# Kernel tuning notes

Hardware: AMD Instinct MI355X
Metric: run time of the kernel (lower is better)

The kernel has to match this reference:

```python
import jax, jax.numpy as jnp
import numpy as np

NUM_HEADS = 16
EMBED_DIM = 1024
HEAD_DIM = EMBED_DIM // NUM_HEADS
REG_LEN = 2048
SUM_LEN = 64
BSZ = 2
REL_DIM = 64
NUM_REL_EMB = 64
MAX_SUMMARY = 64
SCALE = HEAD_DIM ** -0.5


def _ln(x, g, b, eps=1e-5):
    m = jnp.mean(x, axis=-1, keepdims=True)
    v = jnp.mean((x - m) ** 2, axis=-1, keepdims=True)
    return (x - m) * jax.lax.rsqrt(v + eps) * g + b


def setup_inputs() -> dict:
    key = jax.random.key(0)
    ks = jax.random.split(key, 16)
    inp = {}
    inp['reg_x'] = jax.random.normal(ks[0], (REG_LEN, BSZ, EMBED_DIM), jnp.float32)
    inp['sum_token_ids'] = jax.random.randint(ks[1], (BSZ, SUM_LEN), 0, MAX_SUMMARY + 1)
    inp['rel_idx'] = jax.random.randint(ks[2], (BSZ, SUM_LEN + REG_LEN, REG_LEN), 0, NUM_REL_EMB)
    inp['sum_len'] = SUM_LEN
    inp['reg_len'] = REG_LEN
    emb = jax.random.normal(ks[3], (MAX_SUMMARY + 1, EMBED_DIM), jnp.float32) * 0.02
    inp['emb_sum'] = emb.at[0].set(0.0)  # padding_idx = 0
    inp['rel_emb0'] = jax.random.normal(ks[4], (NUM_REL_EMB, REL_DIM), jnp.float32) * 0.02

    def lin(k, din, dout):
        return jax.random.normal(k, (din, dout), jnp.float32) * (1.0 / np.sqrt(din))

    inp['Wq'] = lin(ks[5], EMBED_DIM, EMBED_DIM); inp['bq'] = jnp.zeros((EMBED_DIM,), jnp.float32)
    inp['Wk'] = lin(ks[6], EMBED_DIM, EMBED_DIM); inp['bk'] = jnp.zeros((EMBED_DIM,), jnp.float32)
    inp['Wv'] = lin(ks[7], EMBED_DIM, EMBED_DIM); inp['bv'] = jnp.zeros((EMBED_DIM,), jnp.float32)
    inp['Wr0'] = lin(ks[8], REL_DIM, EMBED_DIM); inp['br0'] = jnp.zeros((EMBED_DIM,), jnp.float32)
    inp['Wk2'] = lin(ks[9], HEAD_DIM, HEAD_DIM); inp['bk2'] = jnp.zeros((HEAD_DIM,), jnp.float32)
    inp['Wv2'] = lin(ks[10], HEAD_DIM, HEAD_DIM); inp['bv2'] = jnp.zeros((HEAD_DIM,), jnp.float32)
    inp['Wo'] = lin(ks[11], EMBED_DIM, EMBED_DIM); inp['bo'] = jnp.zeros((EMBED_DIM,), jnp.float32)
    for name in ['ln_k', 'ln_v', 'ln_k2', 'ln_v2']:
        inp[name + '_g'] = jnp.ones((HEAD_DIM,), jnp.float32)
        inp[name + '_b'] = jnp.zeros((HEAD_DIM,), jnp.float32)
    return inp


def reference(reg_x, sum_token_ids, rel_idx, sum_len, reg_len, emb_sum, rel_emb0,
              Wq, bq, Wk, bk, Wv, bv, Wr0, br0, Wk2, bk2, Wv2, bv2, Wo, bo,
              ln_k_g, ln_k_b, ln_v_g, ln_v_b, ln_k2_g, ln_k2_b, ln_v2_g, ln_v2_b):
    R, B, E = reg_x.shape  # reg_len, bsz, embed_dim
    H, D = NUM_HEADS, HEAD_DIM
    S = sum_token_ids.shape[1]

    # regular K/V projections + per-head LayerNorm
    reg_k = _ln((reg_x @ Wk + bk).reshape(R, B, H, D), ln_k_g, ln_k_b)
    reg_v = _ln((reg_x @ Wv + bv).reshape(R, B, H, D), ln_v_g, ln_v_b)

    # relation-type embedding projection -> [Rrel, H, D]
    r0 = (rel_emb0 @ Wr0 + br0).reshape(NUM_REL_EMB, H, D)

    # --- stage 1: summary tokens attend over regular tokens ---
    sum_x = emb_sum[sum_token_ids.T]                     # [S, B, E]
    sum_q = sum_x.reshape(S, B, H, D) * SCALE
    scores_sum = jnp.einsum('sbhd,kbhd->bhsk', sum_q, reg_k)   # [B,H,S,R]
    qr_sum = jnp.einsum('sbhd,Zhd->bhsZ', sum_q, r0)           # [B,H,S,Rrel]
    idx_sum = rel_idx[:, :S]                                   # [B,S,R]
    scores_sum = scores_sum + jnp.take_along_axis(qr_sum, idx_sum[:, None, :, :], axis=-1)
    w_sum = jax.nn.softmax(scores_sum, axis=-1)
    sum_x2 = jnp.einsum('bhsk,kbhd->sbhd', w_sum, reg_v)       # [S,B,H,D]

    sum_k2 = _ln(sum_x2 @ Wk2 + bk2, ln_k2_g, ln_k2_b)
    sum_v2 = _ln(sum_x2 @ Wv2 + bv2, ln_v2_g, ln_v2_b)

    # --- stage 2: regular tokens attend over [summary ; regular] keys ---
    reg_q = (reg_x @ Wq + bq).reshape(R, B, H, D) * SCALE
    scores_rs = jnp.einsum('qbhd,sbhd->bhqs', reg_q, sum_k2)   # [B,H,R,S]
    scores_rr = jnp.einsum('qbhd,kbhd->bhqk', reg_q, reg_k)    # [B,H,R,R]
    qr_reg = jnp.einsum('qbhd,Zhd->bhqZ', reg_q, r0)
    idx_reg = rel_idx[:, S:]                                   # [B,R,R]
    scores_rr = scores_rr + jnp.take_along_axis(qr_reg, idx_reg[:, None, :, :], axis=-1)
    scores = jnp.concatenate([scores_rs, scores_rr], axis=-1)  # [B,H,R,S+R]
    w = jax.nn.softmax(scores, axis=-1)
    v_all = jnp.concatenate([sum_v2, reg_v], axis=0)           # [S+R,B,H,D]
    attn_out = jnp.einsum('bhqk,kbhd->qbhd', w, v_all).reshape(R, B, E)
    reg_x2 = attn_out @ Wo + bo
    return reg_x2
```

## Files before the change

kernel.cpp:

```cpp
#include <hip/hip_runtime.h>
#include <cstdint>
#include <cstddef>

#define NH   16
#define HD   64
#define RLEN 2048
#define BSZ  2
#define SLEN 64
#define NZ   64
#define ED   1024
#define KTOT 2112
#define NSPLIT 8

typedef __bf16 bf16_t;
typedef bf16_t bf16x8 __attribute__((ext_vector_type(8)));
typedef bf16_t bf16x4 __attribute__((ext_vector_type(4)));
typedef float  f32x4  __attribute__((ext_vector_type(4)));

__device__ __forceinline__ f32x4 mfma16(bf16x8 a, bf16x8 b, f32x4 c) {
    return __builtin_amdgcn_mfma_f32_16x16x32_bf16(a, b, c, 0, 0, 0);
}

__device__ __forceinline__ void dma16(const void* g, void* l) {
    __builtin_amdgcn_global_load_lds(
        (const __attribute__((address_space(1))) unsigned int*)g,
        (__attribute__((address_space(3))) unsigned int*)l, 16, 0, 0);
}


template<int BM>
__global__ __launch_bounds__(256) void gemm_fast(
    const bf16_t* __restrict__ A, const bf16_t* __restrict__ Bt,
    const float* __restrict__ b0, const float* __restrict__ b1,
    const float* __restrict__ b2,
    bf16_t* __restrict__ oq, float* __restrict__ o1, float* __restrict__ o2,
    int M, int K, int N, int mode)
{
    constexpr int MT = BM / 64;
    __shared__ __align__(16) bf16_t As[BM * 64];
    __shared__ __align__(16) bf16_t Bs[128 * 64];

    const int t = threadIdx.x;
    const int wave = t >> 6, lane = t & 63;
    const int quad = lane >> 4, l15 = lane & 15;
    const int rsub = lane >> 3, gq = lane & 7;
    const int m0 = blockIdx.y * BM, n0 = blockIdx.x * 128;

    f32x4 acc[MT][8];
#pragma unroll
    for (int i = 0; i < MT; i++)
#pragma unroll
        for (int j = 0; j < 8; j++) acc[i][j] = (f32x4){0.f, 0.f, 0.f, 0.f};

    for (int k0 = 0; k0 < K; k0 += 64) {
#pragma unroll
        for (int j = 0; j < BM / 32; j++) {
            int row = wave * (BM / 4) + j * 8 + rsub;
            const bf16_t* g = A + (size_t)(m0 + row) * K + k0 + ((gq ^ (row & 7)) * 8);
            dma16(g, As + (wave * (BM / 4) + j * 8) * 64);
        }
#pragma unroll
        for (int j = 0; j < 4; j++) {
            int row = wave * 32 + j * 8 + rsub;
            const bf16_t* g = Bt + (size_t)(n0 + row) * K + k0 + ((gq ^ (row & 7)) * 8);
            dma16(g, Bs + (wave * 32 + j * 8) * 64);
        }
        __syncthreads();

#pragma unroll
        for (int kk = 0; kk < 2; kk++) {
            const int pg = ((kk * 4 + quad) ^ (l15 & 7)) * 8;
            bf16x8 af[MT], bf[8];
#pragma unroll
            for (int mt = 0; mt < MT; mt++)
                af[mt] = *(const bf16x8*)(As + (wave * (BM / 4) + mt * 16 + l15) * 64 + pg);
#pragma unroll
            for (int nt = 0; nt < 8; nt++)
                bf[nt] = *(const bf16x8*)(Bs + (nt * 16 + l15) * 64 + pg);
#pragma unroll
            for (int mt = 0; mt < MT; mt++)
#pragma unroll
                for (int nt = 0; nt < 8; nt++)
                    acc[mt][nt] = mfma16(af[mt], bf[nt], acc[mt][nt]);
        }
        __syncthreads();
    }

#pragma unroll
    for (int mt = 0; mt < MT; mt++)
#pragma unroll
        for (int nt = 0; nt < 8; nt++)
#pragma unroll
            for (int reg = 0; reg < 4; reg++) {
                int m = m0 + wave * (BM / 4) + mt * 16 + quad * 4 + reg;
                int n = n0 + nt * 16 + l15;
                if (mode == 0) {
                    o1[(size_t)m * N + n] = acc[mt][nt][reg] + b0[n];
                } else {
                    int seg = n >> 10, nl = n & 1023;
                    const float* bias = (seg == 0) ? b0 : (seg == 1) ? b1 : b2;
                    float c = acc[mt][nt][reg] + bias[nl];
                    int h = nl >> 6, d = nl & 63;
                    int r = m >> 1, bb = m & 1;
                    size_t off = (((size_t)bb * NH + h) * RLEN + r) * HD + d;
                    if (seg == 0)      oq[off] = (bf16_t)(c * 0.125f);
                    else if (seg == 1) o1[off] = c;
                    else               o2[off] = c;
                }
            }
}

__global__ __launch_bounds__(256) void gemm_mfma(
    const bf16_t* __restrict__ A, const bf16_t* __restrict__ Bt,
    const float* __restrict__ bias, float* __restrict__ outf,
    int M, int K, int N, int Rr)
{
    constexpr int LDA = 40;
    __shared__ __align__(16) bf16_t As[64 * LDA];
    __shared__ __align__(16) bf16_t Bs[128 * LDA];

    const int t = threadIdx.x;
    const int wave = t >> 6, lane = t & 63;
    const int quad = lane >> 4, l15 = lane & 15;
    const int wrow = wave >> 1, wcol = wave & 1;
    const int m0 = blockIdx.y * 64, n0 = blockIdx.x * 128;

    f32x4 acc[2][4];
#pragma unroll
    for (int i = 0; i < 2; i++)
#pragma unroll
        for (int j = 0; j < 4; j++) acc[i][j] = (f32x4){0.f, 0.f, 0.f, 0.f};

    const int srow = t >> 2, sseg = (t & 3) * 8;

    for (int k0 = 0; k0 < K; k0 += 32) {
        bf16x8 av  = *(const bf16x8*)(A  + (size_t)(m0 + srow) * K + k0 + sseg);
        bf16x8 bv0 = *(const bf16x8*)(Bt + (size_t)(n0 + srow) * K + k0 + sseg);
        bf16x8 bv1 = *(const bf16x8*)(Bt + (size_t)(n0 + 64 + srow) * K + k0 + sseg);
        __syncthreads();
        *(bf16x8*)(As + srow * LDA + sseg)        = av;
        *(bf16x8*)(Bs + srow * LDA + sseg)        = bv0;
        *(bf16x8*)(Bs + (64 + srow) * LDA + sseg) = bv1;
        __syncthreads();

        bf16x8 af[2], bf[4];
#pragma unroll
        for (int mt = 0; mt < 2; mt++)
            af[mt] = *(const bf16x8*)(As + (wrow * 32 + mt * 16 + l15) * LDA + quad * 8);
#pragma unroll
        for (int nt = 0; nt < 4; nt++)
            bf[nt] = *(const bf16x8*)(Bs + (wcol * 64 + nt * 16 + l15) * LDA + quad * 8);
#pragma unroll
        for (int mt = 0; mt < 2; mt++)
#pragma unroll
            for (int nt = 0; nt < 4; nt++)
                acc[mt][nt] = mfma16(af[mt], bf[nt], acc[mt][nt]);
    }

#pragma unroll
    for (int mt = 0; mt < 2; mt++)
#pragma unroll
        for (int nt = 0; nt < 4; nt++)
#pragma unroll
            for (int reg = 0; reg < 4; reg++) {
                int m = m0 + wrow * 32 + mt * 16 + quad * 4 + reg;
                int n = n0 + wcol * 64 + nt * 16 + l15;
                if (m >= M) continue;
                float c = acc[mt][nt][reg] + bias[n];
                int h = n >> 6, d = n & 63;
                outf[(((size_t)h) * Rr + m) * HD + d] = c;
            }
}

__global__ __launch_bounds__(256) void ln_k_frag(
    const float* __restrict__ x, const float* __restrict__ g, const float* __restrict__ b,
    bf16_t* __restrict__ kfm)
{
    int row  = blockIdx.x * 4 + (threadIdx.x >> 6);
    int lane = threadIdx.x & 63;
    float v = x[(size_t)row * HD + lane];
    float s1 = v, s2 = v * v;
#pragma unroll
    for (int o = 32; o > 0; o >>= 1) {
        s1 += __shfl_xor(s1, o);
        s2 += __shfl_xor(s2, o);
    }
    float mean = s1 * (1.f / 64.f);
    float var  = s2 * (1.f / 64.f) - mean * mean;
// ... 7 lines not shown

__global__ __launch_bounds__(256) void lnv_frag(
    const float* __restrict__ v, const float* __restrict__ g,
    const float* __restrict__ b, bf16_t* __restrict__ vfm)
{
    __shared__ float tile[64][65];
    const int bh = blockIdx.y, tidx = blockIdx.x;
    const int t = threadIdx.x;
    const int wave = t >> 6, lane = t & 63;

#pragma unroll
    for (int i = 0; i < 16; i++) {
        int rl = wave * 16 + i;
        float x = v[((size_t)bh * RLEN + tidx * 64 + rl) * HD + lane];
        float s1 = x, s2 = x * x;
#pragma unroll
        for (int o = 32; o > 0; o >>= 1) {
            s1 += __shfl_xor(s1, o);
            s2 += __shfl_xor(s2, o);
        }
        float mean = s1 * (1.f / 64.f);
        float var  = s2 * (1.f / 64.f) - mean * mean;
        tile[rl][lane] = (x - mean) * rsqrtf(var + 1e-5f) * g[lane] + b[lane];
    }
    __syncthreads();
    int d = t >> 2, rs = (t & 3) * 16;
    bf16x8 o0, o1;
#pragma unroll
    for (int j = 0; j < 8; j++) {
        o0[j] = (bf16_t)tile[rs + j][d];
        o1[j] = (bf16_t)tile[rs + 8 + j][d];
    }
    size_t base = (size_t)bh * 131072;
    size_t off0 = base + (size_t)((((tidx * 4 + (d >> 4)) * 2 + (rs >> 5)) * 64
                  + ((rs >> 3) & 3) * 16 + (d & 15)) * 8);
    int rs2 = rs + 8;
    size_t off1 = base + (size_t)((((tidx * 4 + (d >> 4)) * 2 + (rs2 >> 5)) * 64
                  + ((rs2 >> 3) & 3) * 16 + (d & 15)) * 8);
    *(bf16x8*)(vfm + off0) = o0;
    *(bf16x8*)(vfm + off1) = o1;
}

__global__ __launch_bounds__(256) void cvt_bf16(
    const float* __restrict__ src, bf16_t* __restrict__ dst, int n)
{
    int i = (blockIdx.x * 256 + threadIdx.x) * 4;
    if (i < n) {
        float4 v = *(const float4*)(src + i);
        bf16x4 o;
        o[0] = (bf16_t)v.x; o[1] = (bf16_t)v.y; o[2] = (bf16_t)v.z; o[3] = (bf16_t)v.w;
        *(bf16x4*)(dst + i) = o;
    }
}

__global__ __launch_bounds__(256) void prep_batch(
    const float* __restrict__ Wq, const float* __restrict__ Wk,
    const float* __restrict__ Wv, const float* __restrict__ Wo,
    const float* __restrict__ Wr0,
    bf16_t* __restrict__ wqt, bf16_t* __restrict__ wkt,
    bf16_t* __restrict__ wvt, bf16_t* __restrict__ wot,
    bf16_t* __restrict__ wr0t,
    const float* __restrict__ emb, const int* __restrict__ ids,
    bf16_t* __restrict__ sum_q,
    const float* __restrict__ rel_emb0, bf16_t* __restrict__ re0b)
{
    const int bid = blockIdx.x;
    const int t = threadIdx.x;

    if (bid >= 1168) {
        int i = ((bid - 1168) * 256 + t) * 4;
        float4 v = *(const float4*)(rel_emb0 + i);
        bf16x4 o;
        o[0] = (bf16_t)v.x; o[1] = (bf16_t)v.y; o[2] = (bf16_t)v.z; o[3] = (bf16_t)v.w;
        *(bf16x4*)(re0b + i) = o;
        return;
    }
    if (bid >= 1040) {
        int sb = bid - 1040;
        int s = sb >> 1, b = sb & 1;
        int id = ids[b * SLEN + s];
        const float* src = emb + (size_t)id * ED;
        for (int e = t; e < ED; e += 256) {
            int h = e >> 6, d = e & 63;
            sum_q[(((size_t)b * NH + h) * SLEN + s) * HD + d] = (bf16_t)(src[e] * 0.125f);
        }
        return;
    }

    __shared__ float tile[64][65];
    const float* src; bf16_t* dst; int R, C, r0, c0;
    if (bid < 1024) {
        int sel = bid >> 8, local = bid & 255;
        src = (sel == 0) ? Wq : (sel == 1) ? Wk : (sel == 2) ? Wv : Wo;
        dst = (sel == 0) ? wqt : (sel == 1) ? wkt : (sel == 2) ? wvt : wot;
        R = ED; C = ED; r0 = (local >> 4) * 64; c0 = (local & 15) * 64;
    } else {
        src = Wr0; dst = wr0t; R = NZ; C = ED; r0 = 0; c0 = (bid - 1024) * 64;
    }
#pragma unroll
    for (int i = 0; i < 4; i++) {
        int idx = t + i * 256;
        int r = idx >> 4, c = (idx & 15) * 4;
        float4 vv = *(const float4*)(src + (size_t)(r0 + r) * C + c0 + c);
        tile[r][c] = vv.x; tile[r][c + 1] = vv.y; tile[r][c + 2] = vv.z; tile[r][c + 3] = vv.w;
    }
    __syncthreads();
    int cc = t >> 2, rs = (t & 3) * 16;
    bf16x8 o0, o1;
#pragma unroll
    for (int j = 0; j < 8; j++) {
        o0[j] = (bf16_t)tile[rs + j][cc];
        o1[j] = (bf16_t)tile[rs + 8 + j][cc];
    }
    *(bf16x8*)(dst + (size_t)(c0 + cc) * R + r0 + rs) = o0;
    *(bf16x8*)(dst + (size_t)(c0 + cc) * R + r0 + rs + 8) = o1;
}

template<int MT>
__device__ __forceinline__ void attn_tile(
    const bf16_t* __restrict__ kt, const bf16_t* __restrict__ vt,
    const int* __restrict__ relbase, int koff, bool userel,
    const float* __restrict__ qrsw, bf16_t* __restrict__ Psw,
    const bf16x8 (&qf)[MT][2],
    f32x4 (&O)[MT][4], float& m_q, float (&l_i)[MT][4],
    int quad, int l15, int lane)
{
    bf16x8 kf[4][2];
#pragma unroll
    for (int nt = 0; nt < 4; nt++)
#pragma unroll
        for (int kb = 0; kb < 2; kb++)
            kf[nt][kb] = *(const bf16x8*)(kt + ((nt * 2 + kb) * 64 + lane) * 8);

    int4 crel[MT][4];
    if (userel) {
#pragma unroll
        for (int mt = 0; mt < MT; mt++)
#pragma unroll
            for (int reg = 0; reg < 4; reg++)
                crel[mt][reg] = *(const int4*)(relbase + (size_t)(mt * 16 + reg) * RLEN + koff);
    }

    f32x4 S[MT][4];
#pragma unroll
    for (int mt = 0; mt < MT; mt++)
#pragma unroll
        for (int nt = 0; nt < 4; nt++) {
            f32x4 acc = (f32x4){0.f, 0.f, 0.f, 0.f};
            acc = mfma16(qf[mt][0], kf[nt][0], acc);
            acc = mfma16(qf[mt][1], kf[nt][1], acc);
            S[mt][nt] = acc;
        }

    bf16x8 vf[4][2];
#pragma unroll
    for (int nt = 0; nt < 4; nt++)
#pragma unroll
        for (int kb = 0; kb < 2; kb++)
            vf[nt][kb] = *(const bf16x8*)(vt + ((nt * 2 + kb) * 64 + lane) * 8);

    if (userel) {
#pragma unroll
        for (int mt = 0; mt < MT; mt++)
#pragma unroll
            for (int reg = 0; reg < 4; reg++) {
                const float* qr = qrsw + (mt * 16 + quad * 4 + reg) * 64;
                int4 c = crel[mt][reg];
                S[mt][0][reg] += qr[c.x];
                S[mt][1][reg] += qr[c.y];
                S[mt][2][reg] += qr[c.z];
                S[mt][3][reg] += qr[c.w];
            }
    }

    float v = -1e30f;
#pragma unroll
    for (int mt = 0; mt < MT; mt++)
#pragma unroll
        for (int nt = 0; nt < 4; nt++) {
            f32x4 s = S[mt][nt];
            v = fmaxf(v, fmaxf(fmaxf(s[0], s[1]), fmaxf(s[2], s[3])));
        }
#pragma unroll
    for (int o = 8; o > 0; o >>= 1) v = fmaxf(v, __shfl_xor(v, o));
    float mnew = fmaxf(m_q, v);
    float alpha = __expf(m_q - mnew);
    m_q = mnew;

#pragma unroll
    for (int mt = 0; mt < MT; mt++)
#pragma unroll
        for (int nt = 0; nt < 4; nt++)
#pragma unroll
            for (int reg = 0; reg < 4; reg++)
                S[mt][nt][reg] = __expf(S[mt][nt][reg] - mnew);

#pragma unroll
    for (int mt = 0; mt < MT; mt++) {
#pragma unroll
        for (int nt = 0; nt < 4; nt++) {
            O[mt][nt][0] *= alpha; O[mt][nt][1] *= alpha;
            O[mt][nt][2] *= alpha; O[mt][nt][3] *= alpha;
        }
#pragma unroll
        for (int reg = 0; reg < 4; reg++) l_i[mt][reg] *= alpha;
    }

    bf16x8 ones;
#pragma unroll
    for (int j = 0; j < 8; j++) ones[j] = (bf16_t)1.0f;

#pragma unroll
    for (int mt = 0; mt < MT; mt++)
#pragma unroll
        for (int reg = 0; reg < 4; reg++) {
            bf16x4 pv;
            pv[0] = (bf16_t)S[mt][0][reg]; pv[1] = (bf16_t)S[mt][1][reg];
            pv[2] = (bf16_t)S[mt][2][reg]; pv[3] = (bf16_t)S[mt][3][reg];
            *(bf16x4*)(Psw + (mt * 16 + quad * 4 + reg) * 72 + 4 * l15) = pv;
        }

#pragma unroll
    for (int mt = 0; mt < MT; mt++) {
        bf16x8 pf0 = *(const bf16x8*)(Psw + (mt * 16 + l15) * 72 + quad * 8);
        bf16x8 pf1 = *(const bf16x8*)(Psw + (mt * 16 + l15) * 72 + 32 + quad * 8);
        f32x4 ls = (f32x4){0.f, 0.f, 0.f, 0.f};
        ls = mfma16(pf0, ones, ls);
        ls = mfma16(pf1, ones, ls);
#pragma unroll
        for (int nt = 0; nt < 4; nt++) {
            O[mt][nt] = mfma16(pf0, vf[nt][0], O[mt][nt]);
            O[mt][nt] = mfma16(pf1, vf[nt][1], O[mt][nt]);
        }
#pragma unroll
        for (int reg = 0; reg < 4; reg++) l_i[mt][reg] += ls[reg];
    }
}

template<int MT>
__device__ __forceinline__ void build_qr(
    const float* __restrict__ r0, int h, const bf16x8 (&qf)[MT][2],
    float* __restrict__ qrsw, int quad, int l15)
{
#pragma unroll
    for (int nt = 0; nt < 4; nt++) {
        const float* rp = r0 + ((size_t)h * NZ + l15 + 16 * nt) * HD + quad * 8;
        float4 a0 = *(const float4*)(rp);
        float4 a1 = *(const float4*)(rp + 4);
        bf16x8 bf0;
        bf0[0] = (bf16_t)a0.x; bf0[1] = (bf16_t)a0.y; bf0[2] = (bf16_t)a0.z; bf0[3] = (bf16_t)a0.w;
        bf0[4] = (bf16_t)a1.x; bf0[5] = (bf16_t)a1.y; bf0[6] = (bf16_t)a1.z; bf0[7] = (bf16_t)a1.w;
        float4 b0 = *(const float4*)(rp + 32);
        float4 b1 = *(const float4*)(rp + 36);
        bf16x8 bf1;
        bf1[0] = (bf16_t)b0.x; bf1[1] = (bf16_t)b0.y; bf1[2] = (bf16_t)b0.z; bf1[3] = (bf16_t)b0.w;
        bf1[4] = (bf16_t)b1.x; bf1[5] = (bf16_t)b1.y; bf1[6] = (bf16_t)b1.z; bf1[7] = (bf16_t)b1.w;
#pragma unroll
        for (int mt = 0; mt < MT; mt++) {
            f32x4 qa = (f32x4){0.f, 0.f, 0.f, 0.f};
            qa = mfma16(qf[mt][0], bf0, qa);
            qa = mfma16(qf[mt][1], bf1, qa);
#pragma unroll
            for (int reg = 0; reg < 4; reg++)
                qrsw[(mt * 16 + quad * 4 + reg) * 64 + l15 + 16 * nt] = qa[reg];
        }
    }
}

__global__ __launch_bounds__(256) void sum_attn_split(
    const bf16_t* __restrict__ Qb,
    const bf16_t* __restrict__ kfm, const bf16_t* __restrict__ vfm,
    const float*  __restrict__ r0,
    const int*    __restrict__ rel_idx,
    float* __restrict__ po, float* __restrict__ pm, float* __restrict__ pl)
{
    const int bh = blockIdx.x;
    const int split = blockIdx.y;
    const int b = bh >> 4, h = bh & 15;
    const int t = threadIdx.x;
    const int wave = t >> 6, lane = t & 63;
    const int quad = lane >> 4, l15 = lane & 15;

    __shared__ __align__(16) bf16_t Ps[4][16 * 72];
    __shared__ float qrs[4][16 * 64];

    bf16x8 qf[1][2];
    const bf16_t* Qrow = Qb + ((size_t)bh * SLEN + wave * 16 + l15) * HD;
    qf[0][0] = *(const bf16x8*)(Qrow + quad * 8);
    qf[0][1] = *(const bf16x8*)(Qrow + 32 + quad * 8);

    build_qr<1>(r0, h, qf, qrs[wave], quad, l15);

    f32x4 O[1][4];
    float m_q = -1e30f;
    float l_i[1][4];
#pragma unroll
    for (int nt = 0; nt < 4; nt++) O[0][nt] = (f32x4){0.f, 0.f, 0.f, 0.f};
#pragma unroll
    for (int r = 0; r < 4; r++) l_i[0][r] = 0.f;

    const int* relbase = rel_idx + ((size_t)b * KTOT + wave * 16 + quad * 4) * RLEN + 4 * l15;

    const bf16_t* kbase = kfm + (size_t)bh * 131072 + (size_t)(split * 4) * 4096;
    const bf16_t* vbase = vfm + (size_t)bh * 131072 + (size_t)(split * 4) * 4096;

    for (int i = 0; i < 4; i++) {
        const int koff = (split * 4 + i) * 64;
        attn_tile<1>(kbase + (size_t)i * 4096, vbase + (size_t)i * 4096,
                     relbase, koff, true, qrs[wave], Ps[wave], qf,
                     O, m_q, l_i, quad, l15, lane);
    }

    const size_t pslot = (size_t)bh * NSPLIT + split;
#pragma unroll
    for (int nt = 0; nt < 4; nt++)
#pragma unroll
        for (int reg = 0; reg < 4; reg++) {
            int sq = wave * 16 + quad * 4 + reg;
            po[(pslot * SLEN + sq) * HD + l15 + 16 * nt] = O[0][nt][reg];
        }
#pragma unroll
    for (int reg = 0; reg < 4; reg++) {
        int sq = wave * 16 + quad * 4 + reg;
        if (l15 == 0) {
            pm[pslot * SLEN + sq] = m_q;
            pl[pslot * SLEN + sq] = l_i[0][reg];
        }
    }
}

__global__ __launch_bounds__(64) void k2v2_fused(
    const float* __restrict__ po, const float* __restrict__ pm,
    const float* __restrict__ pl,
    const float* __restrict__ Wk2, const float* __restrict__ bk2,
    const float* __restrict__ Wv2, const float* __restrict__ bv2,
    const float* __restrict__ gk, const float* __restrict__ bk,
    const float* __restrict__ gv, const float* __restrict__ bv,
    bf16_t* __restrict__ k2fm, bf16_t* __restrict__ v2fm)
{
    int row = blockIdx.x;
    int d = threadIdx.x;
    int bh = row >> 6, s = row & 63;

    float M = -1e30f, mm[NSPLIT];
#pragma unroll
    for (int j = 0; j < NSPLIT; j++) {
        mm[j] = pm[((size_t)bh * NSPLIT + j) * SLEN + s];
        M = fmaxf(M, mm[j]);
    }
    float L = 0.f, acc = 0.f;
#pragma unroll
    for (int j = 0; j < NSPLIT; j++) {
        float a = __expf(mm[j] - M);
        L += pl[((size_t)bh * NSPLIT + j) * SLEN + s] * a;
        acc += po[(((size_t)bh * NSPLIT + j) * SLEN + s) * HD + d] * a;
    }
    __shared__ float xs[64];
    xs[d] = acc / L;
    __syncthreads();

#pragma unroll
    for (int which = 0; which < 2; which++) {
        const float* W  = which ? Wv2 : Wk2;
        const float* bi = which ? bv2 : bk2;
        const float* g  = which ? gv : gk;
        const float* bb = which ? bv : bk;
        float a = bi[d];
#pragma unroll
        for (int j = 0; j < 64; j++) a += xs[j] * W[j * HD + d];
        float s1 = a, s2 = a * a;
#pragma unroll
        for (int o = 32; o > 0; o >>= 1) {
            s1 += __shfl_xor(s1, o);
            s2 += __shfl_xor(s2, o);
        }
        float mean = s1 * (1.f / 64.f);
        float var  = s2 * (1.f / 64.f) - mean * mean;
        float y = (a - mean) * rsqrtf(var + 1e-5f) * g[d] + bb[d];
        if (which == 0) {
            size_t off = (size_t)bh * 4096 +
                (size_t)((((s & 3) * 2 + (d >> 5)) * 64
                          + ((d >> 3) & 3) * 16 + (s >> 2)) * 8 + (d & 7));
            k2fm[off] = (bf16_t)y;
        } else {
            size_t off = (size_t)bh * 4096 +
                (size_t)((((d >> 4) * 2 + (s >> 5)) * 64
                          + ((s >> 3) & 3) * 16 + (d & 15)) * 8 + (s & 7));
            v2fm[off] = (bf16_t)y;
        }
    }
}

__global__ __launch_bounds__(256) void reg_attn_mfma(
    const bf16_t* __restrict__ Qb,
    const bf16_t* __restrict__ kfm, const bf16_t* __restrict__ vfm,
    const bf16_t* __restrict__ k2fm, const bf16_t* __restrict__ v2fm,
    const float*  __restrict__ r0,
    const int*    __restrict__ rel_idx,
    bf16_t* __restrict__ attn_out)
{
    const int bid = blockIdx.x;
    const int bh = (bid & 7) * 4 + ((bid >> 3) & 3);
    const int qt = bid >> 5;
    const int b = bh >> 4, h = bh & 15;
    const int q0 = qt * 128;

    const int t = threadIdx.x;
    const int wave = t >> 6, lane = t & 63;
    const int quad = lane >> 4, l15 = lane & 15;

    __shared__ __align__(16) bf16_t Ps[4][32 * 72];
    __shared__ float qrs[4][32 * 64];

    bf16x8 qf[2][2];
#pragma unroll
    for (int mt = 0; mt < 2; mt++) {
        const bf16_t* Qrow = Qb + ((size_t)bh * RLEN + q0 + wave * 32 + mt * 16 + l15) * HD;
        qf[mt][0] = *(const bf16x8*)(Qrow + quad * 8);
        qf[mt][1] = *(const bf16x8*)(Qrow + 32 + quad * 8);
    }

    build_qr<2>(r0, h, qf, qrs[wave], quad, l15);

    f32x4 O[2][4];
    float m_q = -1e30f;
    float l_i[2][4];
#pragma unroll
    for (int mt = 0; mt < 2; mt++)
#pragma unroll
        for (int nt = 0; nt < 4; nt++) O[mt][nt] = (f32x4){0.f, 0.f, 0.f, 0.f};
#pragma unroll
    for (int mt = 0; mt < 2; mt++)
#pragma unroll
        for (int r = 0; r < 4; r++) l_i[mt][r] = 0.f;

    const int* relbase = rel_idx +
        ((size_t)b * KTOT + SLEN + q0 + wave * 32 + quad * 4) * RLEN + 4 * l15;

    attn_tile<2>(k2fm + (size_t)bh * 4096, v2fm + (size_t)bh * 4096,
                 relbase, 0, false, qrs[wave], Ps[wave], qf,
                 O, m_q, l_i, quad, l15, lane);

    const bf16_t* kt = kfm + (size_t)bh * 131072;
    const bf16_t* vt = vfm + (size_t)bh * 131072;
    for (int tile = 0; tile < 32; tile++) {
        attn_tile<2>(kt, vt, relbase, tile * 64, true,
                     qrs[wave], Ps[wave], qf, O, m_q, l_i, quad, l15, lane);
        kt += 4096; vt += 4096;
    }

#pragma unroll
    for (int mt = 0; mt < 2; mt++) {
        float linv[4];
#pragma unroll
        for (int reg = 0; reg < 4; reg++) linv[reg] = 1.0f / l_i[mt][reg];
#pragma unroll
        for (int nt = 0; nt < 4; nt++)
#pragma unroll
            for (int reg = 0; reg < 4; reg++) {
                int q = q0 + wave * 32 + mt * 16 + quad * 4 + reg;
                attn_out[((size_t)q * BSZ + b) * ED + h * HD + l15 + 16 * nt] =
                    (bf16_t)(O[mt][nt][reg] * linv[reg]);
            }
    }
}

extern "C" void kernel_launch(void* const* d_in, const int* in_sizes, int n_in,
                              void* d_out, int out_size, void* d_ws, size_t ws_size,
                              hipStream_t stream)
{
    const float* reg_x    = (const float*)d_in[0];
    const int*   sum_ids  = (const int*)d_in[1];
    const int*   rel_idx  = (const int*)d_in[2];
    const float* emb_sum  = (const float*)d_in[5];
    const float* rel_emb0 = (const float*)d_in[6];
    const float* Wq = (const float*)d_in[7];
    const float* bq = (const float*)d_in[8];
    const float* Wk = (const float*)d_in[9];
    const float* bk = (const float*)d_in[10];
    const float* Wv = (const float*)d_in[11];
    const float* bv = (const float*)d_in[12];
    const float* Wr0 = (const float*)d_in[13];
    const float* br0 = (const float*)d_in[14];
    const float* Wk2 = (const float*)d_in[15];
    const float* bk2 = (const float*)d_in[16];
    const float* Wv2 = (const float*)d_in[17];
    const float* bv2 = (const float*)d_in[18];
    const float* Wo  = (const float*)d_in[19];
    const float* bo  = (const float*)d_in[20];
    const float* ln_k_g  = (const float*)d_in[21];
    const float* ln_k_b  = (const float*)d_in[22];
    const float* ln_v_g  = (const float*)d_in[23];
    const float* ln_v_b  = (const float*)d_in[24];
    const float* ln_k2_g = (const float*)d_in[25];
    const float* ln_k2_b = (const float*)d_in[26];
    const float* ln_v2_g = (const float*)d_in[27];
    const float* ln_v2_b = (const float*)d_in[28];

    const size_t QKV = (size_t)BSZ * NH * RLEN * HD;
    const size_t SUM = (size_t)BSZ * NH * SLEN * HD;

    float* ws  = (float*)d_ws;
    float* k   = ws;
    float* v   = k + QKV;
    float* r0  = v + QKV;

    bf16_t* xb   = (bf16_t*)(r0 + (size_t)NH * NZ * HD);
    bf16_t* qb   = xb + QKV;
    bf16_t* kfm  = qb + QKV;
    bf16_t* vfm  = kfm + QKV;
    bf16_t* sqb  = vfm + QKV;
    bf16_t* k2fm = sqb + SUM;
    bf16_t* v2fm = k2fm + SUM;
    bf16_t* wqt  = v2fm + SUM;
    bf16_t* wkt  = wqt + (size_t)ED * ED;
    bf16_t* wvt  = wkt + (size_t)ED * ED;
    bf16_t* wot  = wvt + (size_t)ED * ED;
    bf16_t* wr0t = wot + (size_t)ED * ED;
    bf16_t* re0b = wr0t + (size_t)ED * NZ;
    bf16_t* aob  = (bf16_t*)k;
    float*  po   = (float*)xb;
    float*  pm   = po + (size_t)BSZ * NH * NSPLIT * SLEN * HD;
    float*  pl   = pm + (size_t)BSZ * NH * NSPLIT * SLEN;

    const int M = RLEN * BSZ;

    cvt_bf16<<<(int)(QKV / 1024), 256, 0, stream>>>(reg_x, xb, (int)QKV);
    prep_batch<<<1172, 256, 0, stream>>>(Wq, Wk, Wv, Wo, Wr0,
                                         wqt, wkt, wvt, wot, wr0t,
                                         emb_sum, sum_ids, sqb, rel_emb0, re0b);

    gemm_fast<128><<<dim3(3 * ED / 128, M / 128), 256, 0, stream>>>(
        xb, wqt, bq, bk, bv, qb, k, v, M, ED, 3 * ED, 1);

    ln_k_frag<<<(BSZ * NH * RLEN) / 4, 256, 0, stream>>>(k, ln_k_g, ln_k_b, kfm);
    lnv_frag<<<dim3(RLEN / 64, BSZ * NH), 256, 0, stream>>>(v, ln_v_g, ln_v_b, vfm);

    gemm_mfma<<<dim3(ED / 128, 1), 256, 0, stream>>>(re0b, wr0t, br0, r0, NZ, NZ, ED, NZ);

    sum_attn_split<<<dim3(BSZ * NH, NSPLIT), 256, 0, stream>>>(sqb, kfm, vfm, r0, rel_idx, po, pm, pl);

    k2v2_fused<<<BSZ * NH * SLEN, 64, 0, stream>>>(po, pm, pl, Wk2, bk2, Wv2, bv2,
                                                   ln_k2_g, ln_k2_b, ln_v2_g, ln_v2_b,
                                                   k2fm, v2fm);

    reg_attn_mfma<<<512, 256, 0, stream>>>(qb, kfm, vfm, k2fm, v2fm, r0, rel_idx, aob);

    gemm_fast<64><<<dim3(ED / 128, M / 64), 256, 0, stream>>>(
        aob, wot, bo, nullptr, nullptr, nullptr, (float*)d_out, nullptr, M, ED, ED, 0);
}
```

Measured before the change: 371.0 us.

## Use exp2 softmax with lazy rescaling and finer-grained attention work split

The log2(e) factor is folded into the query scale so that all softmax exponentials use exp2f. The running-max rescale of O and l is skipped when the new tile max stays within 8 of the current max. The regular-attention kernel drops to one 16-row M tile per wave and launches twice as many blocks. The summary attention split count is doubled from 8 to 16, and its partial buffers move into the v workspace to make room. The aim is cheaper exponentials, less rescaling work and better GPU occupancy, at the cost of more K/V reloads per query and larger bf16 P values, up to 256, under lazy rescaling.

```diff
diff --git a/kernel.cpp b/kernel.cpp
--- a/kernel.cpp
+++ b/kernel.cpp
@@ -10,7 +10,9 @@
 #define NZ   64
 #define ED   1024
 #define KTOT 2112
-#define NSPLIT 8
+#define NSPLIT 16
+
+#define QSCALE 0.18033688011112042f
 
 typedef __bf16 bf16_t;
 typedef bf16_t bf16x8 __attribute__((ext_vector_type(8)));
@@ -103,7 +105,7 @@
                     int h = nl >> 6, d = nl & 63;
                     int r = m >> 1, bb = m & 1;
                     size_t off = (((size_t)bb * NH + h) * RLEN + r) * HD + d;
-                    if (seg == 0)      oq[off] = (bf16_t)(c * 0.125f);
+                    if (seg == 0)      oq[off] = (bf16_t)(c * QSCALE);
                     else if (seg == 1) o1[off] = c;
                     else               o2[off] = c;
                 }
@@ -277,7 +279,7 @@
         const float* src = emb + (size_t)id * ED;
         for (int e = t; e < ED; e += 256) {
             int h = e >> 6, d = e & 63;
-            sum_q[(((size_t)b * NH + h) * SLEN + s) * HD + d] = (bf16_t)(src[e] * 0.125f);
+            sum_q[(((size_t)b * NH + h) * SLEN + s) * HD + d] = (bf16_t)(src[e] * QSCALE);
         }
         return;
     }
@@ -378,9 +380,22 @@
         }
 #pragma unroll
     for (int o = 8; o > 0; o >>= 1) v = fmaxf(v, __shfl_xor(v, o));
-    float mnew = fmaxf(m_q, v);
-    float alpha = __expf(m_q - mnew);
-    m_q = mnew;
+
+    if (!__all(v <= m_q + 8.0f)) {
+        float mnew = fmaxf(m_q, v);
+        float alpha = exp2f(m_q - mnew);
+        m_q = mnew;
+#pragma unroll
+        for (int mt = 0; mt < MT; mt++) {
+#pragma unroll
+            for (int nt = 0; nt < 4; nt++) {
+                O[mt][nt][0] *= alpha; O[mt][nt][1] *= alpha;
+                O[mt][nt][2] *= alpha; O[mt][nt][3] *= alpha;
+            }
+#pragma unroll
+            for (int reg = 0; reg < 4; reg++) l_i[mt][reg] *= alpha;
+        }
+    }
 
 #pragma unroll
     for (int mt = 0; mt < MT; mt++)
@@ -388,18 +403,7 @@
         for (int nt = 0; nt < 4; nt++)
 #pragma unroll
             for (int reg = 0; reg < 4; reg++)
-                S[mt][nt][reg] = __expf(S[mt][nt][reg] - mnew);
-
-#pragma unroll
-    for (int mt = 0; mt < MT; mt++) {
-#pragma unroll
-        for (int nt = 0; nt < 4; nt++) {
-            O[mt][nt][0] *= alpha; O[mt][nt][1] *= alpha;
-            O[mt][nt][2] *= alpha; O[mt][nt][3] *= alpha;
-        }
-#pragma unroll
-        for (int reg = 0; reg < 4; reg++) l_i[mt][reg] *= alpha;
-    }
+                S[mt][nt][reg] = exp2f(S[mt][nt][reg] - m_q);
 
     bf16x8 ones;
 #pragma unroll
@@ -469,6 +473,7 @@
     const int*    __restrict__ rel_idx,
     float* __restrict__ po, float* __restrict__ pm, float* __restrict__ pl)
 {
+    constexpr int TPS = 32 / NSPLIT;
     const int bh = blockIdx.x;
     const int split = blockIdx.y;
     const int b = bh >> 4, h = bh & 15;
@@ -496,11 +501,11 @@
 
     const int* relbase = rel_idx + ((size_t)b * KTOT + wave * 16 + quad * 4) * RLEN + 4 * l15;
 
-    const bf16_t* kbase = kfm + (size_t)bh * 131072 + (size_t)(split * 4) * 4096;
-    const bf16_t* vbase = vfm + (size_t)bh * 131072 + (size_t)(split * 4) * 4096;
-
-    for (int i = 0; i < 4; i++) {
-        const int koff = (split * 4 + i) * 64;
+    const bf16_t* kbase = kfm + (size_t)bh * 131072 + (size_t)(split * TPS) * 4096;
+    const bf16_t* vbase = vfm + (size_t)bh * 131072 + (size_t)(split * TPS) * 4096;
+
+    for (int i = 0; i < TPS; i++) {
+        const int koff = (split * TPS + i) * 64;
         attn_tile<1>(kbase + (size_t)i * 4096, vbase + (size_t)i * 4096,
                      relbase, koff, true, qrs[wave], Ps[wave], qf,
                      O, m_q, l_i, quad, l15, lane);
@@ -546,7 +551,7 @@
     float L = 0.f, acc = 0.f;
 #pragma unroll
     for (int j = 0; j < NSPLIT; j++) {
-        float a = __expf(mm[j] - M);
+        float a = exp2f(mm[j] - M);
         L += pl[((size_t)bh * NSPLIT + j) * SLEN + s] * a;
         acc += po[(((size_t)bh * NSPLIT + j) * SLEN + s) * HD + d] * a;
     }
@@ -598,64 +603,58 @@
     const int bh = (bid & 7) * 4 + ((bid >> 3) & 3);
     const int qt = bid >> 5;
     const int b = bh >> 4, h = bh & 15;
-    const int q0 = qt * 128;
+    const int q0 = qt * 64;
 
     const int t = threadIdx.x;
     const int wave = t >> 6, lane = t & 63;
     const int quad = lane >> 4, l15 = lane & 15;
 
-    __shared__ __align__(16) bf16_t Ps[4][32 * 72];
-    __shared__ float qrs[4][32 * 64];
-
-    bf16x8 qf[2][2];
-#pragma unroll
-    for (int mt = 0; mt < 2; mt++) {
-        const bf16_t* Qrow = Qb + ((size_t)bh * RLEN + q0 + wave * 32 + mt * 16 + l15) * HD;
-        qf[mt][0] = *(const bf16x8*)(Qrow + quad * 8);
-        qf[mt][1] = *(const bf16x8*)(Qrow + 32 + quad * 8);
-    }
-
-    build_qr<2>(r0, h, qf, qrs[wave], quad, l15);
-
-    f32x4 O[2][4];
+    __shared__ __align__(16) bf16_t Ps[4][16 * 72];
+    __shared__ float qrs[4][16 * 64];
+
+    bf16x8 qf[1][2];
+    {
+        const bf16_t* Qrow = Qb + ((size_t)bh * RLEN + q0 + wave * 16 + l15) * HD;
+        qf[0][0] = *(const bf16x8*)(Qrow + quad * 8);
+        qf[0][1] = *(const bf16x8*)(Qrow + 32 + quad * 8);
+    }
+
+    build_qr<1>(r0, h, qf, qrs[wave], quad, l15);
+
+    f32x4 O[1][4];
     float m_q = -1e30f;
-    float l_i[2][4];
-#pragma unroll
-    for (int mt = 0; mt < 2; mt++)
-#pragma unroll
-        for (int nt = 0; nt < 4; nt++) O[mt][nt] = (f32x4){0.f, 0.f, 0.f, 0.f};
-#pragma unroll
-    for (int mt = 0; mt < 2; mt++)
-#pragma unroll
-        for (int r = 0; r < 4; r++) l_i[mt][r] = 0.f;
+    float l_i[1][4];
+#pragma unroll
+    for (int nt = 0; nt < 4; nt++) O[0][nt] = (f32x4){0.f, 0.f, 0.f, 0.f};
+#pragma unroll
+    for (int r = 0; r < 4; r++) l_i[0][r] = 0.f;
 
     const int* relbase = rel_idx +
-        ((size_t)b * KTOT + SLEN + q0 + wave * 32 + quad * 4) * RLEN + 4 * l15;
-
-    attn_tile<2>(k2fm + (size_t)bh * 4096, v2fm + (size_t)bh * 4096,
+        ((size_t)b * KTOT + SLEN + q0 + wave * 16 + quad * 4) * RLEN + 4 * l15;
+
+    attn_tile<1>(k2fm + (size_t)bh * 4096, v2fm + (size_t)bh * 4096,
                  relbase, 0, false, qrs[wave], Ps[wave], qf,
                  O, m_q, l_i, quad, l15, lane);
 
     const bf16_t* kt = kfm + (size_t)bh * 131072;
     const bf16_t* vt = vfm + (size_t)bh * 131072;
     for (int tile = 0; tile < 32; tile++) {
-        attn_tile<2>(kt, vt, relbase, tile * 64, true,
+        attn_tile<1>(kt, vt, relbase, tile * 64, true,
                      qrs[wave], Ps[wave], qf, O, m_q, l_i, quad, l15, lane);
         kt += 4096; vt += 4096;
     }
 
-#pragma unroll
-    for (int mt = 0; mt < 2; mt++) {
+    {
         float linv[4];
 #pragma unroll
-        for (int reg = 0; reg < 4; reg++) linv[reg] = 1.0f / l_i[mt][reg];
+        for (int reg = 0; reg < 4; reg++) linv[reg] = 1.0f / l_i[0][reg];
 #pragma unroll
         for (int nt = 0; nt < 4; nt++)
 #pragma unroll
             for (int reg = 0; reg < 4; reg++) {
-                int q = q0 + wave * 32 + mt * 16 + quad * 4 + reg;
+                int q = q0 + wave * 16 + quad * 4 + reg;
                 attn_out[((size_t)q * BSZ + b) * ED + h * HD + l15 + 16 * nt] =
-                    (bf16_t)(O[mt][nt][reg] * linv[reg]);
+                    (bf16_t)(O[0][nt][reg] * linv[reg]);
             }
     }
 }
@@ -714,7 +713,7 @@
     bf16_t* wr0t = wot + (size_t)ED * ED;
     bf16_t* re0b = wr0t + (size_t)ED * NZ;
     bf16_t* aob  = (bf16_t*)k;
-    float*  po   = (float*)xb;
+    float*  po   = v;
     float*  pm   = po + (size_t)BSZ * NH * NSPLIT * SLEN * HD;
     float*  pl   = pm + (size_t)BSZ * NH * NSPLIT * SLEN;
 
@@ -739,7 +738,7 @@
                                                    ln_k2_g, ln_k2_b, ln_v2_g, ln_v2_b,
                                                    k2fm, v2fm);
 
-    reg_attn_mfma<<<512, 256, 0, stream>>>(qb, kfm, vfm, k2fm, v2fm, r0, rel_idx, aob);
+    reg_attn_mfma<<<1024, 256, 0, stream>>>(qb, kfm, vfm, k2fm, v2fm, r0, rel_idx, aob);
 
     gemm_fast<64><<<dim3(ED / 128, M / 64), 256, 0, stream>>>(
         aob, wot, bo, nullptr, nullptr, nullptr, (float*)d_out, nullptr, M, ED, ED, 0);
```

Result: slower. 398.6 us (+7.4%).

## Split KV range across wave halves in reg attention and use exp2 lazy rescale

Applied to the files above, without the earlier changes.

The regular-token attention kernel now runs 8 waves per block. Two halves each process half of the key tiles for the same queries, then merge their partial max, sum and output through shared memory. Softmax switches to exp2, with log2(e) folded into the query scale, and skips rescaling of the accumulators when the running max grows by at most 8. The summary-attention split count doubles to 16, and its partial buffers move into the freed v workspace. These changes aim to raise parallelism and cut exp and rescale work, at the cost of extra block syncs, more shared memory and register pressure under the 512-thread launch bound.

```diff
diff --git a/kernel.cpp b/kernel.cpp
--- a/kernel.cpp
+++ b/kernel.cpp
@@ -10,7 +10,9 @@
 #define NZ   64
 #define ED   1024
 #define KTOT 2112
-#define NSPLIT 8
+#define NSPLIT 16
+
+#define QSCALE 0.18033688011112042f
 
 typedef __bf16 bf16_t;
 typedef bf16_t bf16x8 __attribute__((ext_vector_type(8)));
@@ -103,7 +105,7 @@
                     int h = nl >> 6, d = nl & 63;
                     int r = m >> 1, bb = m & 1;
                     size_t off = (((size_t)bb * NH + h) * RLEN + r) * HD + d;
-                    if (seg == 0)      oq[off] = (bf16_t)(c * 0.125f);
+                    if (seg == 0)      oq[off] = (bf16_t)(c * QSCALE);
                     else if (seg == 1) o1[off] = c;
                     else               o2[off] = c;
                 }
@@ -277,7 +279,7 @@
         const float* src = emb + (size_t)id * ED;
         for (int e = t; e < ED; e += 256) {
             int h = e >> 6, d = e & 63;
-            sum_q[(((size_t)b * NH + h) * SLEN + s) * HD + d] = (bf16_t)(src[e] * 0.125f);
+            sum_q[(((size_t)b * NH + h) * SLEN + s) * HD + d] = (bf16_t)(src[e] * QSCALE);
         }
         return;
     }
@@ -378,9 +380,22 @@
         }
 #pragma unroll
     for (int o = 8; o > 0; o >>= 1) v = fmaxf(v, __shfl_xor(v, o));
-    float mnew = fmaxf(m_q, v);
-    float alpha = __expf(m_q - mnew);
-    m_q = mnew;
+
+    if (!__all(v <= m_q + 8.0f)) {
+        float mnew = fmaxf(m_q, v);
+        float alpha = exp2f(m_q - mnew);
+        m_q = mnew;
+#pragma unroll
+        for (int mt = 0; mt < MT; mt++) {
+#pragma unroll
+            for (int nt = 0; nt < 4; nt++) {
+                O[mt][nt][0] *= alpha; O[mt][nt][1] *= alpha;
+                O[mt][nt][2] *= alpha; O[mt][nt][3] *= alpha;
+            }
+#pragma unroll
+            for (int reg = 0; reg < 4; reg++) l_i[mt][reg] *= alpha;
+        }
+    }
 
 #pragma unroll
     for (int mt = 0; mt < MT; mt++)
@@ -388,18 +403,7 @@
         for (int nt = 0; nt < 4; nt++)
 #pragma unroll
             for (int reg = 0; reg < 4; reg++)
-                S[mt][nt][reg] = __expf(S[mt][nt][reg] - mnew);
-
-#pragma unroll
-    for (int mt = 0; mt < MT; mt++) {
-#pragma unroll
-        for (int nt = 0; nt < 4; nt++) {
-            O[mt][nt][0] *= alpha; O[mt][nt][1] *= alpha;
-            O[mt][nt][2] *= alpha; O[mt][nt][3] *= alpha;
-        }
-#pragma unroll
-        for (int reg = 0; reg < 4; reg++) l_i[mt][reg] *= alpha;
-    }
+                S[mt][nt][reg] = exp2f(S[mt][nt][reg] - m_q);
 
     bf16x8 ones;
 #pragma unroll
@@ -469,6 +473,7 @@
     const int*    __restrict__ rel_idx,
     float* __restrict__ po, float* __restrict__ pm, float* __restrict__ pl)
 {
+    constexpr int TPS = 32 / NSPLIT;
     const int bh = blockIdx.x;
     const int split = blockIdx.y;
     const int b = bh >> 4, h = bh & 15;
@@ -496,11 +501,11 @@
 
     const int* relbase = rel_idx + ((size_t)b * KTOT + wave * 16 + quad * 4) * RLEN + 4 * l15;
 
-    const bf16_t* kbase = kfm + (size_t)bh * 131072 + (size_t)(split * 4) * 4096;
-    const bf16_t* vbase = vfm + (size_t)bh * 131072 + (size_t)(split * 4) * 4096;
-
-    for (int i = 0; i < 4; i++) {
-        const int koff = (split * 4 + i) * 64;
+    const bf16_t* kbase = kfm + (size_t)bh * 131072 + (size_t)(split * TPS) * 4096;
+    const bf16_t* vbase = vfm + (size_t)bh * 131072 + (size_t)(split * TPS) * 4096;
+
+    for (int i = 0; i < TPS; i++) {
+        const int koff = (split * TPS + i) * 64;
         attn_tile<1>(kbase + (size_t)i * 4096, vbase + (size_t)i * 4096,
                      relbase, koff, true, qrs[wave], Ps[wave], qf,
                      O, m_q, l_i, quad, l15, lane);
@@ -546,7 +551,7 @@
     float L = 0.f, acc = 0.f;
 #pragma unroll
     for (int j = 0; j < NSPLIT; j++) {
-        float a = __expf(mm[j] - M);
+        float a = exp2f(mm[j] - M);
         L += pl[((size_t)bh * NSPLIT + j) * SLEN + s] * a;
         acc += po[(((size_t)bh * NSPLIT + j) * SLEN + s) * HD + d] * a;
     }
@@ -586,7 +591,7 @@
     }
 }
 
-__global__ __launch_bounds__(256) void reg_attn_mfma(
+__global__ __launch_bounds__(512, 4) void reg_attn_mfma(
     const bf16_t* __restrict__ Qb,
     const bf16_t* __restrict__ kfm, const bf16_t* __restrict__ vfm,
     const bf16_t* __restrict__ k2fm, const bf16_t* __restrict__ v2fm,
@@ -602,20 +607,22 @@
 
     const int t = threadIdx.x;
     const int wave = t >> 6, lane = t & 63;
+    const int wq = wave & 3, half = wave >> 2;
     const int quad = lane >> 4, l15 = lane & 15;
 
-    __shared__ __align__(16) bf16_t Ps[4][32 * 72];
-    __shared__ float qrs[4][32 * 64];
+    __shared__ __align__(16) bf16_t Ps[8][32 * 72];
+    __shared__ __align__(16) float qrs[4][32 * 64];
+    __shared__ float msh[2][4][4];
 
     bf16x8 qf[2][2];
 #pragma unroll
     for (int mt = 0; mt < 2; mt++) {
-        const bf16_t* Qrow = Qb + ((size_t)bh * RLEN + q0 + wave * 32 + mt * 16 + l15) * HD;
+        const bf16_t* Qrow = Qb + ((size_t)bh * RLEN + q0 + wq * 32 + mt * 16 + l15) * HD;
         qf[mt][0] = *(const bf16x8*)(Qrow + quad * 8);
         qf[mt][1] = *(const bf16x8*)(Qrow + 32 + quad * 8);
     }
 
-    build_qr<2>(r0, h, qf, qrs[wave], quad, l15);
+    build_qr<2>(r0, h, qf, qrs[wq], quad, l15);
 
     f32x4 O[2][4];
     float m_q = -1e30f;
@@ -630,33 +637,65 @@
         for (int r = 0; r < 4; r++) l_i[mt][r] = 0.f;
 
     const int* relbase = rel_idx +
-        ((size_t)b * KTOT + SLEN + q0 + wave * 32 + quad * 4) * RLEN + 4 * l15;
-
-    attn_tile<2>(k2fm + (size_t)bh * 4096, v2fm + (size_t)bh * 4096,
-                 relbase, 0, false, qrs[wave], Ps[wave], qf,
-                 O, m_q, l_i, quad, l15, lane);
-
-    const bf16_t* kt = kfm + (size_t)bh * 131072;
-    const bf16_t* vt = vfm + (size_t)bh * 131072;
-    for (int tile = 0; tile < 32; tile++) {
-        attn_tile<2>(kt, vt, relbase, tile * 64, true,
-                     qrs[wave], Ps[wave], qf, O, m_q, l_i, quad, l15, lane);
+        ((size_t)b * KTOT + SLEN + q0 + wq * 32 + quad * 4) * RLEN + 4 * l15;
+
+    if (half == 0)
+        attn_tile<2>(k2fm + (size_t)bh * 4096, v2fm + (size_t)bh * 4096,
+                     relbase, 0, false, qrs[wq], Ps[wave], qf,
+                     O, m_q, l_i, quad, l15, lane);
+
+    const bf16_t* kt = kfm + (size_t)bh * 131072 + (size_t)(half * 16) * 4096;
+    const bf16_t* vt = vfm + (size_t)bh * 131072 + (size_t)(half * 16) * 4096;
+    for (int tile = 0; tile < 16; tile++) {
+        attn_tile<2>(kt, vt, relbase, (half * 16 + tile) * 64, true,
+                     qrs[wq], Ps[wave], qf, O, m_q, l_i, quad, l15, lane);
         kt += 4096; vt += 4096;
     }
 
-#pragma unroll
-    for (int mt = 0; mt < 2; mt++) {
-        float linv[4];
-#pragma unroll
-        for (int reg = 0; reg < 4; reg++) linv[reg] = 1.0f / l_i[mt][reg];
-#pragma unroll
-        for (int nt = 0; nt < 4; nt++)
-#pragma unroll
-            for (int reg = 0; reg < 4; reg++) {
-                int q = q0 + wave * 32 + mt * 16 + quad * 4 + reg;
-                attn_out[((size_t)q * BSZ + b) * ED + h * HD + l15 + 16 * nt] =
-                    (bf16_t)(O[mt][nt][reg] * linv[reg]);
-            }
+    msh[half][wq][quad] = m_q;
+    __syncthreads();
+    float mo = msh[1 - half][wq][quad];
+    float al = exp2f(m_q - fmaxf(m_q, mo));
+
+    if (half == 1) {
+        float* osh = qrs[wq];
+        float* lsh = (float*)(Ps[4 + wq]);
+#pragma unroll
+        for (int mt = 0; mt < 2; mt++) {
+#pragma unroll
+            for (int nt = 0; nt < 4; nt++)
+#pragma unroll
+                for (int reg = 0; reg < 4; reg++)
+                    osh[(mt * 16 + quad * 4 + reg) * 64 + l15 + 16 * nt] =
+                        O[mt][nt][reg] * al;
+            if (l15 == 0)
+#pragma unroll
+                for (int reg = 0; reg < 4; reg++)
+                    lsh[mt * 16 + quad * 4 + reg] = l_i[mt][reg] * al;
+        }
+    }
+    __syncthreads();
+    if (half == 0) {
+        const float* osh = qrs[wq];
+        const float* lsh = (const float*)(Ps[4 + wq]);
+#pragma unroll
+        for (int mt = 0; mt < 2; mt++) {
+            float linv[4];
+#pragma unroll
+            for (int reg = 0; reg < 4; reg++)
+                linv[reg] = 1.0f /
+                    (l_i[mt][reg] * al + lsh[mt * 16 + quad * 4 + reg]);
+#pragma unroll
+            for (int nt = 0; nt < 4; nt++)
+#pragma unroll
+                for (int reg = 0; reg < 4; reg++) {
+                    int q = q0 + wq * 32 + mt * 16 + quad * 4 + reg;
+                    float ot = O[mt][nt][reg] * al
+                             + osh[(mt * 16 + quad * 4 + reg) * 64 + l15 + 16 * nt];
+                    attn_out[((size_t)q * BSZ + b) * ED + h * HD + l15 + 16 * nt] =
+                        (bf16_t)(ot * linv[reg]);
+                }
+        }
     }
 }
 
@@ -714,7 +753,7 @@
     bf16_t* wr0t = wot + (size_t)ED * ED;
     bf16_t* re0b = wr0t + (size_t)ED * NZ;
     bf16_t* aob  = (bf16_t*)k;
-    float*  po   = (float*)xb;
+    float*  po   = v;
     float*  pm   = po + (size_t)BSZ * NH * NSPLIT * SLEN * HD;
     float*  pl   = pm + (size_t)BSZ * NH * NSPLIT * SLEN;
 
@@ -739,7 +778,7 @@
                                                    ln_k2_g, ln_k2_b, ln_v2_g, ln_v2_b,
                                                    k2fm, v2fm);
 
-    reg_attn_mfma<<<512, 256, 0, stream>>>(qb, kfm, vfm, k2fm, v2fm, r0, rel_idx, aob);
+    reg_attn_mfma<<<512, 512, 0, stream>>>(qb, kfm, vfm, k2fm, v2fm, r0, rel_idx, aob);
 
     gemm_fast<64><<<dim3(ED / 128, M / 64), 256, 0, stream>>>(
         aob, wot, bo, nullptr, nullptr, nullptr, (float*)d_out, nullptr, M, ED, ED, 0);
```

After: 480.3 us. 29.4% more time.

## Use exp2 softmax with lazy rescale, finer sum splits, single-wave reg attention blocks

Applied to the files above, without the earlier changes.

The softmax now works in base 2: log2(e) is folded into the query scale so exp2f replaces __expf, and the split-merge step is updated to match. The online-softmax rescale of O and l is skipped unless the running max grows by more than 8, which cuts per-tile multiplies and exp calls. The summary attention split count doubles from 8 to 16, with partials moved to the larger fp32 v buffer so they fit. Regular attention launches 2048 single-wave blocks of 32 queries instead of 512 four-wave blocks. This gives more independent blocks for scheduling, at the cost of more blocks each reloading the same K/V tiles.

```diff
diff --git a/kernel.cpp b/kernel.cpp
--- a/kernel.cpp
+++ b/kernel.cpp
@@ -10,7 +10,9 @@
 #define NZ   64
 #define ED   1024
 #define KTOT 2112
-#define NSPLIT 8
+#define NSPLIT 16
+
+#define QSCALE 0.18033688011112042f
 
 typedef __bf16 bf16_t;
 typedef bf16_t bf16x8 __attribute__((ext_vector_type(8)));
@@ -103,7 +105,7 @@
                     int h = nl >> 6, d = nl & 63;
                     int r = m >> 1, bb = m & 1;
                     size_t off = (((size_t)bb * NH + h) * RLEN + r) * HD + d;
-                    if (seg == 0)      oq[off] = (bf16_t)(c * 0.125f);
+                    if (seg == 0)      oq[off] = (bf16_t)(c * QSCALE);
                     else if (seg == 1) o1[off] = c;
                     else               o2[off] = c;
                 }
@@ -277,7 +279,7 @@
         const float* src = emb + (size_t)id * ED;
         for (int e = t; e < ED; e += 256) {
             int h = e >> 6, d = e & 63;
-            sum_q[(((size_t)b * NH + h) * SLEN + s) * HD + d] = (bf16_t)(src[e] * 0.125f);
+            sum_q[(((size_t)b * NH + h) * SLEN + s) * HD + d] = (bf16_t)(src[e] * QSCALE);
         }
         return;
     }
@@ -378,9 +380,22 @@
         }
 #pragma unroll
     for (int o = 8; o > 0; o >>= 1) v = fmaxf(v, __shfl_xor(v, o));
-    float mnew = fmaxf(m_q, v);
-    float alpha = __expf(m_q - mnew);
-    m_q = mnew;
+
+    if (!__all(v <= m_q + 8.0f)) {
+        float mnew = fmaxf(m_q, v);
+        float alpha = exp2f(m_q - mnew);
+        m_q = mnew;
+#pragma unroll
+        for (int mt = 0; mt < MT; mt++) {
+#pragma unroll
+            for (int nt = 0; nt < 4; nt++) {
+                O[mt][nt][0] *= alpha; O[mt][nt][1] *= alpha;
+                O[mt][nt][2] *= alpha; O[mt][nt][3] *= alpha;
+            }
+#pragma unroll
+            for (int reg = 0; reg < 4; reg++) l_i[mt][reg] *= alpha;
+        }
+    }
 
 #pragma unroll
     for (int mt = 0; mt < MT; mt++)
@@ -388,18 +403,7 @@
         for (int nt = 0; nt < 4; nt++)
 #pragma unroll
             for (int reg = 0; reg < 4; reg++)
-                S[mt][nt][reg] = __expf(S[mt][nt][reg] - mnew);
-
-#pragma unroll
-    for (int mt = 0; mt < MT; mt++) {
-#pragma unroll
-        for (int nt = 0; nt < 4; nt++) {
-            O[mt][nt][0] *= alpha; O[mt][nt][1] *= alpha;
-            O[mt][nt][2] *= alpha; O[mt][nt][3] *= alpha;
-        }
-#pragma unroll
-        for (int reg = 0; reg < 4; reg++) l_i[mt][reg] *= alpha;
-    }
+                S[mt][nt][reg] = exp2f(S[mt][nt][reg] - m_q);
 
     bf16x8 ones;
 #pragma unroll
@@ -469,6 +473,7 @@
     const int*    __restrict__ rel_idx,
     float* __restrict__ po, float* __restrict__ pm, float* __restrict__ pl)
 {
+    constexpr int TPS = 32 / NSPLIT;
     const int bh = blockIdx.x;
     const int split = blockIdx.y;
     const int b = bh >> 4, h = bh & 15;
@@ -496,11 +501,11 @@
 
     const int* relbase = rel_idx + ((size_t)b * KTOT + wave * 16 + quad * 4) * RLEN + 4 * l15;
 
-    const bf16_t* kbase = kfm + (size_t)bh * 131072 + (size_t)(split * 4) * 4096;
-    const bf16_t* vbase = vfm + (size_t)bh * 131072 + (size_t)(split * 4) * 4096;
-
-    for (int i = 0; i < 4; i++) {
-        const int koff = (split * 4 + i) * 64;
+    const bf16_t* kbase = kfm + (size_t)bh * 131072 + (size_t)(split * TPS) * 4096;
+    const bf16_t* vbase = vfm + (size_t)bh * 131072 + (size_t)(split * TPS) * 4096;
+
+    for (int i = 0; i < TPS; i++) {
+        const int koff = (split * TPS + i) * 64;
         attn_tile<1>(kbase + (size_t)i * 4096, vbase + (size_t)i * 4096,
                      relbase, koff, true, qrs[wave], Ps[wave], qf,
                      O, m_q, l_i, quad, l15, lane);
@@ -546,7 +551,7 @@
     float L = 0.f, acc = 0.f;
 #pragma unroll
     for (int j = 0; j < NSPLIT; j++) {
-        float a = __expf(mm[j] - M);
+        float a = exp2f(mm[j] - M);
         L += pl[((size_t)bh * NSPLIT + j) * SLEN + s] * a;
         acc += po[(((size_t)bh * NSPLIT + j) * SLEN + s) * HD + d] * a;
     }
@@ -586,7 +591,7 @@
     }
 }
 
-__global__ __launch_bounds__(256) void reg_attn_mfma(
+__global__ __launch_bounds__(64) void reg_attn_mfma(
     const bf16_t* __restrict__ Qb,
     const bf16_t* __restrict__ kfm, const bf16_t* __restrict__ vfm,
     const bf16_t* __restrict__ k2fm, const bf16_t* __restrict__ v2fm,
@@ -598,24 +603,23 @@
     const int bh = (bid & 7) * 4 + ((bid >> 3) & 3);
     const int qt = bid >> 5;
     const int b = bh >> 4, h = bh & 15;
-    const int q0 = qt * 128;
-
-    const int t = threadIdx.x;
-    const int wave = t >> 6, lane = t & 63;
+    const int q0 = qt * 32;
+
+    const int lane = threadIdx.x & 63;
     const int quad = lane >> 4, l15 = lane & 15;
 
-    __shared__ __align__(16) bf16_t Ps[4][32 * 72];
-    __shared__ float qrs[4][32 * 64];
+    __shared__ __align__(16) bf16_t Ps[32 * 72];
+    __shared__ float qrs[32 * 64];
 
     bf16x8 qf[2][2];
 #pragma unroll
     for (int mt = 0; mt < 2; mt++) {
-        const bf16_t* Qrow = Qb + ((size_t)bh * RLEN + q0 + wave * 32 + mt * 16 + l15) * HD;
+        const bf16_t* Qrow = Qb + ((size_t)bh * RLEN + q0 + mt * 16 + l15) * HD;
         qf[mt][0] = *(const bf16x8*)(Qrow + quad * 8);
         qf[mt][1] = *(const bf16x8*)(Qrow + 32 + quad * 8);
     }
 
-    build_qr<2>(r0, h, qf, qrs[wave], quad, l15);
+    build_qr<2>(r0, h, qf, qrs, quad, l15);
 
     f32x4 O[2][4];
     float m_q = -1e30f;
@@ -630,17 +634,17 @@
         for (int r = 0; r < 4; r++) l_i[mt][r] = 0.f;
 
     const int* relbase = rel_idx +
-        ((size_t)b * KTOT + SLEN + q0 + wave * 32 + quad * 4) * RLEN + 4 * l15;
+        ((size_t)b * KTOT + SLEN + q0 + quad * 4) * RLEN + 4 * l15;
 
     attn_tile<2>(k2fm + (size_t)bh * 4096, v2fm + (size_t)bh * 4096,
-                 relbase, 0, false, qrs[wave], Ps[wave], qf,
+                 relbase, 0, false, qrs, Ps, qf,
                  O, m_q, l_i, quad, l15, lane);
 
     const bf16_t* kt = kfm + (size_t)bh * 131072;
     const bf16_t* vt = vfm + (size_t)bh * 131072;
     for (int tile = 0; tile < 32; tile++) {
         attn_tile<2>(kt, vt, relbase, tile * 64, true,
-                     qrs[wave], Ps[wave], qf, O, m_q, l_i, quad, l15, lane);
+                     qrs, Ps, qf, O, m_q, l_i, quad, l15, lane);
         kt += 4096; vt += 4096;
     }
 
@@ -653,7 +657,7 @@
         for (int nt = 0; nt < 4; nt++)
 #pragma unroll
             for (int reg = 0; reg < 4; reg++) {
-                int q = q0 + wave * 32 + mt * 16 + quad * 4 + reg;
+                int q = q0 + mt * 16 + quad * 4 + reg;
                 attn_out[((size_t)q * BSZ + b) * ED + h * HD + l15 + 16 * nt] =
                     (bf16_t)(O[mt][nt][reg] * linv[reg]);
             }
@@ -714,7 +718,7 @@
     bf16_t* wr0t = wot + (size_t)ED * ED;
     bf16_t* re0b = wr0t + (size_t)ED * NZ;
     bf16_t* aob  = (bf16_t*)k;
-    float*  po   = (float*)xb;
+    float*  po   = v;
     float*  pm   = po + (size_t)BSZ * NH * NSPLIT * SLEN * HD;
     float*  pl   = pm + (size_t)BSZ * NH * NSPLIT * SLEN;
 
@@ -739,7 +743,7 @@
                                                    ln_k2_g, ln_k2_b, ln_v2_g, ln_v2_b,
                                                    k2fm, v2fm);
 
-    reg_attn_mfma<<<512, 256, 0, stream>>>(qb, kfm, vfm, k2fm, v2fm, r0, rel_idx, aob);
+    reg_attn_mfma<<<2048, 64, 0, stream>>>(qb, kfm, vfm, k2fm, v2fm, r0, rel_idx, aob);
 
     gemm_fast<64><<<dim3(ED / 128, M / 64), 256, 0, stream>>>(
         aob, wot, bo, nullptr, nullptr, nullptr, (float*)d_out, nullptr, M, ED, ED, 0);
```

New measurement: 391.0 us. +5.4%, slower.
